# Performance work log

Measured on AMD Instinct MI355X. Metric: run time of the kernel, lower is better.

## Reference

```python
import jax, jax.numpy as jnp
import numpy as np
import math

LOG_EPS = -1000.0   # matches LOG_EPS in the torch source
NEG = -1e9          # stand-in for -inf (grad-safe)
T_MIN, T_MAX = 0.1, 1.0
GUMBEL_RATIO = 0.5  # gumbel_temperature_ratio forward arg (scalar float)


def setup_inputs() -> dict:
    key = jax.random.key(0)
    k1, k2, k3 = jax.random.split(key, 3)
    B, I, J, D = 4, 96, 384, 256
    return {
        "text_embeddings": jax.random.normal(k1, (B, I, D), jnp.float32),
        "mel_embeddings": jax.random.normal(k2, (B, J, D), jnp.float32),
        "gumbel_noise_u": jax.random.uniform(k3, (B, I, J), jnp.float32,
                                             minval=1e-6, maxval=1.0 - 1e-6),
        "text_mask": jnp.ones((B, I), dtype=bool),
        "mel_mask": jnp.ones((B, J), dtype=bool),
    }


def _soft_alignment(text_embeddings, mel_embeddings, gumbel_noise_u, text_mask, mel_mask):
    B, I, Dt = text_embeddings.shape
    _, J, Dm = mel_embeddings.shape

    # energy (B, I, J) = bmm / sqrt(D_text * D_mel)
    energy = jnp.einsum('bid,bjd->bij', text_embeddings, mel_embeddings) / math.sqrt(Dt * Dm)
    # gumbel noise + temperature
    temperature = T_MIN + (T_MAX - T_MIN) * GUMBEL_RATIO
    noise = -jnp.log(-jnp.log(gumbel_noise_u))
    energy = (energy + noise) / temperature

    len_t = text_mask.sum(1)  # (B,)
    len_m = mel_mask.sum(1)   # (B,)
    j_idx = jnp.arange(J)

    # invalid triangular mask (B, I, J, K): boundary j must not precede previous boundary k
    tri = j_idx[:, None] < j_idx[None, :]                       # (J, K)
    invalid = (tri[None, None]
               | ~text_mask[:, :, None, None]
               | ~mel_mask[:, None, :, None]
               | ~mel_mask[:, None, None, :])
    # force_assign_last: last text token's boundary forced to the last mel frame
    last_i = jnp.arange(I)[None, :] == (len_t - 1)[:, None]     # (B, I)
    not_last_j = j_idx[None, :] != (len_m - 1)[:, None]         # (B, J)
    invalid = invalid | (last_i[:, :, None, None] & not_last_j[:, None, :, None])

    # log conditional prob P(B_i = j | B_{i-1} = k), normalized over j (axis=2)
    e4 = jnp.where(invalid, LOG_EPS, energy[..., None])         # (B, I, J, K)
    log_cond_prob = e4 - jax.nn.logsumexp(e4, axis=2, keepdims=True)
    # reverse logcumsumexp over j: log P(B_i >= j | B_{i-1} = k)
    geq = jnp.flip(jax.lax.cumlogsumexp(jnp.flip(log_cond_prob, 2), axis=2), 2)
    geq = jnp.where(invalid, LOG_EPS, geq)

    # forward DP: B_ij (B, I+1, J+1), B_ij[:,0,0] = 0
    row0 = jnp.full((B, J + 1), NEG).at[:, 0].set(0.0)
    jj = jnp.arange(1, J + 1)

    def step(prev, inp):
        i, lcp = inp                                            # lcp: (B, J, K=J)
        # B_ij[b,i,j] = lse_k B_ij[b,i-1,k] + log_cond_prob[b,i-1,j-1,k]
        vals = jax.nn.logsumexp(prev[:, None, :-1] + lcp, axis=2)  # (B, J)
        window = (jj >= i) & (jj <= J - I + i + 1)              # only j in [i, J-I+i+1] written
        new = jnp.where(window[None, :], vals, NEG)
        new = jnp.concatenate([jnp.full((B, 1), NEG), new], axis=1)
        return new, new

    _, rows = jax.lax.scan(step, row0,
                           (jnp.arange(1, I + 1), jnp.swapaxes(log_cond_prob, 0, 1)))
    Bij = jnp.concatenate([row0[:, None, :], jnp.swapaxes(rows, 0, 1)], axis=1)  # (B, I+1, J+1)

    prob = Bij[:, :-1, :-1]                                     # (B, I, K)
    # log P(B_{i-1} < j <= B_i) = lse_k prob[b,i,k] + geq[b,i,j,k]
    log_boundary = jax.nn.logsumexp(prob[:, :, None, :] + geq, axis=3)  # (B, I, J)
    return log_boundary


def reference(text_embeddings, mel_embeddings, gumbel_noise_u, text_mask, mel_mask):
    soft = _soft_alignment(text_embeddings, mel_embeddings, gumbel_noise_u,
                           text_mask, mel_mask)
    # expanded text embeddings (B, J, D_text)
    expanded = jnp.einsum('bij,bid->bjd', jnp.exp(soft), text_embeddings)
    return soft, expanded
```

## Files before the change

### kernel.cpp

```cpp
#include <hip/hip_runtime.h>
#include <hip/hip_bf16.h>
#include <math.h>

#define B_ 4
#define I_ 96
#define J_ 384
#define D_ 256
#define NEG_     -1000000000.0f
#define NEGINF_  -3.0e38f
#define INV_TEMP_ (1.0f/0.55f)
#define LOG2E_   1.4426950408889634f
#define LN2_     0.6931471805599453f
#define LOGEPS2_ (-1000.0f*LOG2E_)

__device__ __forceinline__ float lse2(float a, float b) {
    float m = fmaxf(a, b);
    float d = fminf(a, b) - m;
    return m + __log2f(1.0f + __builtin_exp2f(d));
}

template<int CTRL, int RMASK = 0xF>
__device__ __forceinline__ float dpp_mv(float x, float fill) {
    return __int_as_float(__builtin_amdgcn_update_dpp(
        __float_as_int(fill), __float_as_int(x), CTRL, RMASK, 0xF, false));
}
template<int CTRL, int RMASK = 0xF>
__device__ __forceinline__ float dpp_id(float x) { return dpp_mv<CTRL,RMASK>(x, NEGINF_); }
__device__ __forceinline__ float rdlane(float x, int l_const) {
    return __int_as_float(__builtin_amdgcn_readlane(__float_as_int(x), l_const));
}

__device__ __forceinline__ void pcomb(float& m, float& s, float om, float os) {
    float d  = om - m;
    float e  = __builtin_exp2f(-__builtin_fabsf(d));
    float sh = (d > 0.0f) ? os : s;
    float sl = (d > 0.0f) ? s  : os;
    s = __builtin_fmaf(sl, e, sh);
    m = fmaxf(m, om);
}
__device__ __forceinline__ void wave_prefix_pair(float& m, float& s) {
    { float om=dpp_mv<0x111>(m,NEGINF_), os=dpp_mv<0x111>(s,0.f); pcomb(m,s,om,os); }
    { float om=dpp_mv<0x112>(m,NEGINF_), os=dpp_mv<0x112>(s,0.f); pcomb(m,s,om,os); }
    { float om=dpp_mv<0x114>(m,NEGINF_), os=dpp_mv<0x114>(s,0.f); pcomb(m,s,om,os); }
    { float om=dpp_mv<0x118>(m,NEGINF_), os=dpp_mv<0x118>(s,0.f); pcomb(m,s,om,os); }
    { float om=dpp_mv<0x142,0xa>(m,NEGINF_), os=dpp_mv<0x142,0xa>(s,0.f); pcomb(m,s,om,os); }
    { float om=dpp_mv<0x143,0xc>(m,NEGINF_), os=dpp_mv<0x143,0xc>(s,0.f); pcomb(m,s,om,os); }
}

__device__ __forceinline__ float wave_incl_prefix_lse(float x) {
    x = lse2(x, dpp_id<0x111>(x));
    x = lse2(x, dpp_id<0x112>(x));
    x = lse2(x, dpp_id<0x114>(x));
    x = lse2(x, dpp_id<0x118>(x));
    x = lse2(x, dpp_id<0x142, 0xa>(x));
    x = lse2(x, dpp_id<0x143, 0xc>(x));
    return x;
}
__device__ __forceinline__ float wave_incl_suffix_lse(float x, int lane) {
    x = lse2(x, dpp_id<0x101>(x));
    x = lse2(x, dpp_id<0x102>(x));
    x = lse2(x, dpp_id<0x104>(x));
    x = lse2(x, dpp_id<0x108>(x));
    float t1 = rdlane(x, 16), t2 = rdlane(x, 32), t3 = rdlane(x, 48);
    int row = lane >> 4;
    float u23 = lse2(t2, t3);
    float add = (row == 3) ? NEGINF_ : (row == 2) ? t3
              : (row == 1) ? u23 : lse2(t1, u23);
    return lse2(x, add);
}
__device__ __forceinline__ float combine_pre(const float* p, int w) {
    float l01 = lse2(p[0], p[1]);
    float l23 = lse2(p[2], p[3]);
    float P3 = lse2(l01, p[2]);
    float P4 = lse2(l01, l23);
    float P5 = lse2(P4, p[4]);
    return (w == 0) ? NEGINF_ : (w == 1) ? p[0] : (w == 2) ? l01
         : (w == 3) ? P3 : (w == 4) ? P4 : P5;
}
__device__ __forceinline__ float combine_suf(const float* s, int w) {
    float h45 = lse2(s[4], s[5]);
    float h23 = lse2(s[2], s[3]);
    float S3 = lse2(s[3], h45);
    float S2 = lse2(h23, h45);
    float S1 = lse2(s[1], S2);
    return (w == 5) ? NEGINF_ : (w == 4) ? s[5] : (w == 3) ? h45
         : (w == 2) ? S3 : (w == 1) ? S2 : S1;
}

__global__ __launch_bounds__(384) void k_energy(
    const float* __restrict__ text, const float* __restrict__ mel,
    const float* __restrict__ gum, float* __restrict__ Sarr,
    float* __restrict__ Earr)
{
    const int ib = blockIdx.x * 6, b = blockIdx.y;
    const int tid = threadIdx.x, lane = tid & 63, w = tid >> 6;
    __shared__ float4 tex4[6][D_/4];
    __shared__ float e2l[6][J_];

    {
        int r = tid >> 6, c = tid & 63;
        tex4[r][c] = ((const float4*)(text + ((size_t)b*I_ + ib + r)*D_))[c];
    }
    __syncthreads();

    const int j = tid;
    const float4* mrow = (const float4*)(mel + ((size_t)b*J_ + j)*D_);
    float acc[6] = {0.f,0.f,0.f,0.f,0.f,0.f};
    #pragma unroll 4
    for (int d4 = 0; d4 < D_/4; ++d4) {
        float4 m4 = mrow[d4];
        #pragma unroll
        for (int r = 0; r < 6; ++r) {
            float4 t4 = tex4[r][d4];
            acc[r] += t4.x*m4.x + t4.y*m4.y + t4.z*m4.z + t4.w*m4.w;
        }
    }
    #pragma unroll
    for (int r = 0; r < 6; ++r) {
        float u = gum[((size_t)b*I_ + ib + r)*J_ + j];
        float noise = -__logf(-__logf(u));
        e2l[r][j] = (acc[r] * (1.0f/256.0f) + noise) * (INV_TEMP_ * LOG2E_);
    }
    __syncthreads();

    const int k0 = lane * 6;
    float x[6];
    #pragma unroll
    for (int t = 0; t < 6; ++t) x[t] = e2l[w][k0 + t];
    float s1[6], s2[6], sfx[6];
    #pragma unroll
    for (int t = 0; t < 5; ++t) s1[t] = lse2(x[t], x[t+1]);
    s1[5] = x[5];
    #pragma unroll
    for (int t = 0; t < 4; ++t) s2[t] = lse2(s1[t], s1[t+2]);
    s2[4] = s1[4]; s2[5] = s1[5];
    sfx[0] = lse2(s2[0], s2[4]);
    sfx[1] = lse2(s2[1], s2[5]);
    #pragma unroll
    for (int t = 2; t < 6; ++t) sfx[t] = s2[t];
    float incl = wave_incl_suffix_lse(sfx[0], lane);
    float excl = dpp_id<0x130>(incl);
    size_t rowoff = ((size_t)b*I_ + ib + w)*J_ + k0;
    #pragma unroll
    for (int t = 0; t < 6; ++t) {
        Sarr[rowoff + t] = lse2(sfx[t], excl);
        Earr[rowoff + t] = x[t];
    }
}

__global__ __launch_bounds__(64) void k_dp(
    const float* __restrict__ Sarr, const float* __restrict__ Earr,
    float* __restrict__ prob)
{
    const int b = blockIdx.x;
    const int lane = threadIdx.x;
    const int k0 = lane * 6;
    const float* Sb = Sarr + (size_t)b*I_*J_;
    const float* Eb = Earr + (size_t)b*I_*J_;
    float* Pb = prob + (size_t)b*I_*J_;

    float prev[6];
    #pragma unroll
    for (int t = 0; t < 6; ++t) {
        int k = k0 + t;
        float v0 = (k == 0) ? 0.0f : NEG_;
        prev[t] = v0;
        Pb[k] = v0;
    }
    float SA[6], EA[6], SBf[6], EBf[6];
    #pragma unroll
    for (int t = 0; t < 6; ++t) {
        int k = k0 + t;
        SA[t] = Sb[k];
        EA[t] = Eb[(k == 0) ? 0 : k - 1];
    }
    #pragma unroll
    for (int t = 0; t < 6; ++t) {
        int k = k0 + t;
        SBf[t] = Sb[(size_t)1*J_ + k];
        EBf[t] = Eb[(size_t)1*J_ + ((k == 0) ? 0 : k - 1)];
    }

    auto STEP = [&](int i, float* Sx, float* Ex, int loadrow) {
        float v[6], E6[6];
        #pragma unroll
        for (int t = 0; t < 6; ++t) { v[t] = prev[t] - Sx[t]; E6[t] = Ex[t]; }
        if (loadrow >= 0) {
            #pragma unroll
            for (int t = 0; t < 6; ++t) {
                int k = k0 + t;
                Sx[t] = Sb[(size_t)loadrow*J_ + k];
                Ex[t] = Eb[(size_t)loadrow*J_ + ((k == 0) ? 0 : k - 1)];
            }
        }
        float qm[6], qs[6];
        qm[0] = v[0]; qs[0] = 1.0f;
        #pragma unroll
        for (int t = 1; t < 6; ++t) { qm[t] = v[t]; qs[t] = 1.0f; pcomb(qm[t], qs[t], v[t-1], 1.0f); }
        float rm[6], rs[6];
        rm[0] = qm[0]; rs[0] = qs[0]; rm[1] = qm[1]; rs[1] = qs[1];
        #pragma unroll
        for (int t = 2; t < 6; ++t) { rm[t] = qm[t]; rs[t] = qs[t]; pcomb(rm[t], rs[t], qm[t-2], qs[t-2]); }
        float fm[6], fs[6];
        #pragma unroll
        for (int t = 0; t < 4; ++t) { fm[t] = rm[t]; fs[t] = rs[t]; }
        fm[4] = rm[4]; fs[4] = rs[4]; pcomb(fm[4], fs[4], rm[0], rs[0]);
        fm[5] = rm[5]; fs[5] = rs[5]; pcomb(fm[5], fs[5], rm[1], rs[1]);
        float Lm = fm[5], Ls = fs[5];
        wave_prefix_pair(Lm, Ls);
        float pexm = dpp_mv<0x138>(Lm, NEGINF_);
        float pexs = dpp_mv<0x138>(Ls, 0.0f);
        float nv[6];
        nv[0] = pexm + __log2f(pexs) + E6[0];
        #pragma unroll
        for (int t = 1; t < 6; ++t) {
            float cm = pexm, cs = pexs;
            pcomb(cm, cs, fm[t-1], fs[t-1]);
            nv[t] = cm + __log2f(cs) + E6[t];
        }
        float* Prow = Pb + (size_t)i*J_;
        #pragma unroll
        for (int t = 0; t < 6; ++t) {
            int k = k0 + t;
            bool win = (k >= i) && (k <= 289 + i);
            float val = win ? nv[t] : NEG_;
            prev[t] = val;
            Prow[k] = val;
        }
    };

    int i = 1;
    for (; i + 1 <= I_-1; i += 2) {
        STEP(i,     SA,  EA,  (i + 1 <= I_-2) ? i + 1 : -1);
        STEP(i + 1, SBf, EBf, (i + 2 <= I_-2) ? i + 2 : -1);
    }
    if (i == I_-1) STEP(i, SA, EA, -1);
}

__global__ __launch_bounds__(384) void k_soft(
    float* __restrict__ probsoft,
    const float* __restrict__ Sarr)
{
    const int i = blockIdx.x, b = blockIdx.y;
    const int tid = threadIdx.x, lane = tid & 63, w = tid >> 6;
    const int j = tid;
    __shared__ float tot[12];
    float* Row = probsoft + ((size_t)b*I_ + i)*J_;
    float p = Row[j];

    if (i == I_-1) {
        float sincl = wave_incl_suffix_lse(p, lane);
        if (lane == 0) tot[w] = sincl;
        __syncthreads();
        float m = tot[0];
        #pragma unroll
        for (int t = 1; t < 6; ++t) m = lse2(m, tot[t]);
        Row[j] = (j == J_-1) ? LN2_ * m : LN2_ * m - 1000.0f;
        return;
    }

    float S6 = Sarr[((size_t)b*I_ + i)*J_ + j];
    float v = p - S6;
    float qincl = wave_incl_prefix_lse(v);
    float tsuf  = wave_incl_suffix_lse(p, lane);
    if (lane == 63) tot[w] = qincl;
    if (lane == 0)  tot[6 + w] = tsuf;
    __syncthreads();
    float pt[6], st[6];
    #pragma unroll
    for (int t = 0; t < 6; ++t) { pt[t] = tot[t]; st[t] = tot[6+t]; }
    float Qful = lse2(combine_pre(pt, w), qincl);
    float Texw = dpp_id<0x130>(tsuf);
    float Texc = lse2(combine_suf(st, w), Texw);
    Row[j] = LN2_ * lse2(Qful + S6, Texc + LOGEPS2_);
}

__global__ __launch_bounds__(256) void k_expand(
    const float* __restrict__ soft, const float* __restrict__ text,
    float* __restrict__ out2)
{
    const int jb = blockIdx.x * 8, b = blockIdx.y;
    const int tid = threadIdx.x;
    __shared__ float wsh[8][I_];
    for (int n = tid; n < 8*I_; n += 256) {
        int jj = n / I_, ii = n % I_;
        wsh[jj][ii] = __expf(soft[((size_t)b*I_ + ii)*J_ + jb + jj]);
    }
    __syncthreads();
    float acc[8] = {0.f,0.f,0.f,0.f,0.f,0.f,0.f,0.f};
    const float* tcol = text + (size_t)b*I_*D_ + tid;
    #pragma unroll 4
    for (int ii = 0; ii < I_; ++ii) {
        float tv = tcol[(size_t)ii*D_];
        #pragma unroll
        for (int jj = 0; jj < 8; ++jj) acc[jj] += wsh[jj][ii] * tv;
    }
    #pragma unroll
    for (int jj = 0; jj < 8; ++jj)
        out2[((size_t)b*J_ + jb + jj)*D_ + tid] = acc[jj];
}

extern "C" void kernel_launch(void* const* d_in, const int* in_sizes, int n_in,
                              void* d_out, int out_size, void* d_ws, size_t ws_size,
                              hipStream_t stream) {
    const float* text = (const float*)d_in[0];
    const float* mel  = (const float*)d_in[1];
    const float* gum  = (const float*)d_in[2];

    float* out    = (float*)d_out;
    float* soft   = out;
    float* out2   = out + (size_t)B_*I_*J_;
    float* Sarr   = out2;
    float* Earr   = out2 + (size_t)B_*I_*J_;
    float* prob   = soft;

    k_energy<<<dim3(I_/6, B_), 384, 0, stream>>>(text, mel, gum, Sarr, Earr);
    k_dp    <<<dim3(B_),        64, 0, stream>>>(Sarr, Earr, prob);
    k_soft  <<<dim3(I_, B_),   384, 0, stream>>>(prob, Sarr);
    k_expand<<<dim3(J_/8, B_), 256, 0, stream>>>(soft, text, out2);
}
```

Before: 163.6 us.

## Fuse DP recursion and soft-boundary pass into one kernel with LDS-resident probabilities

Merges the single-wave DP kernel and the per-row soft-alignment kernel into one 384-thread block per batch. The full probability table (96x384 floats) stays in shared memory, which removes a kernel launch and the global write/read round-trip of the prob rows. Wave 0 runs the DP while the other waves idle; after a barrier all six waves compute the soft output, 16 rows each. The DP scan also switches from a (max, scaled-sum) pair combine to plain pairwise log-sum-exp, which needs a log per combine but carries fewer values. The soft phase now runs on only 4 blocks instead of 384, so that work is serialized.

```diff
diff --git a/kernel.cpp b/kernel.cpp
--- a/kernel.cpp
+++ b/kernel.cpp
@@ -20,31 +20,12 @@
 }
 
 template<int CTRL, int RMASK = 0xF>
-__device__ __forceinline__ float dpp_mv(float x, float fill) {
+__device__ __forceinline__ float dpp_id(float x) {
     return __int_as_float(__builtin_amdgcn_update_dpp(
-        __float_as_int(fill), __float_as_int(x), CTRL, RMASK, 0xF, false));
-}
-template<int CTRL, int RMASK = 0xF>
-__device__ __forceinline__ float dpp_id(float x) { return dpp_mv<CTRL,RMASK>(x, NEGINF_); }
+        __float_as_int(NEGINF_), __float_as_int(x), CTRL, RMASK, 0xF, false));
+}
 __device__ __forceinline__ float rdlane(float x, int l_const) {
     return __int_as_float(__builtin_amdgcn_readlane(__float_as_int(x), l_const));
-}
-
-__device__ __forceinline__ void pcomb(float& m, float& s, float om, float os) {
-    float d  = om - m;
-    float e  = __builtin_exp2f(-__builtin_fabsf(d));
-    float sh = (d > 0.0f) ? os : s;
-    float sl = (d > 0.0f) ? s  : os;
-    s = __builtin_fmaf(sl, e, sh);
-    m = fmaxf(m, om);
-}
-__device__ __forceinline__ void wave_prefix_pair(float& m, float& s) {
-    { float om=dpp_mv<0x111>(m,NEGINF_), os=dpp_mv<0x111>(s,0.f); pcomb(m,s,om,os); }
-    { float om=dpp_mv<0x112>(m,NEGINF_), os=dpp_mv<0x112>(s,0.f); pcomb(m,s,om,os); }
-    { float om=dpp_mv<0x114>(m,NEGINF_), os=dpp_mv<0x114>(s,0.f); pcomb(m,s,om,os); }
-    { float om=dpp_mv<0x118>(m,NEGINF_), os=dpp_mv<0x118>(s,0.f); pcomb(m,s,om,os); }
-    { float om=dpp_mv<0x142,0xa>(m,NEGINF_), os=dpp_mv<0x142,0xa>(s,0.f); pcomb(m,s,om,os); }
-    { float om=dpp_mv<0x143,0xc>(m,NEGINF_), os=dpp_mv<0x143,0xc>(s,0.f); pcomb(m,s,om,os); }
 }
 
 __device__ __forceinline__ float wave_incl_prefix_lse(float x) {
@@ -68,24 +49,6 @@
               : (row == 1) ? u23 : lse2(t1, u23);
     return lse2(x, add);
 }
-__device__ __forceinline__ float combine_pre(const float* p, int w) {
-    float l01 = lse2(p[0], p[1]);
-    float l23 = lse2(p[2], p[3]);
-    float P3 = lse2(l01, p[2]);
-    float P4 = lse2(l01, l23);
-    float P5 = lse2(P4, p[4]);
-    return (w == 0) ? NEGINF_ : (w == 1) ? p[0] : (w == 2) ? l01
-         : (w == 3) ? P3 : (w == 4) ? P4 : P5;
-}
-__device__ __forceinline__ float combine_suf(const float* s, int w) {
-    float h45 = lse2(s[4], s[5]);
-    float h23 = lse2(s[2], s[3]);
-    float S3 = lse2(s[3], h45);
-    float S2 = lse2(h23, h45);
-    float S1 = lse2(s[1], S2);
-    return (w == 5) ? NEGINF_ : (w == 4) ? s[5] : (w == 3) ? h45
-         : (w == 2) ? S3 : (w == 1) ? S2 : S1;
-}
 
 __global__ __launch_bounds__(384) void k_energy(
     const float* __restrict__ text, const float* __restrict__ mel,
@@ -148,131 +111,154 @@
     }
 }
 
-__global__ __launch_bounds__(64) void k_dp(
+__global__ __launch_bounds__(384) void k_dpsoft(
     const float* __restrict__ Sarr, const float* __restrict__ Earr,
-    float* __restrict__ prob)
+    float* __restrict__ soft)
 {
+    __shared__ float probL[I_*J_];
     const int b = blockIdx.x;
-    const int lane = threadIdx.x;
+    const int tid = threadIdx.x, lane = tid & 63, w = tid >> 6;
     const int k0 = lane * 6;
     const float* Sb = Sarr + (size_t)b*I_*J_;
-    const float* Eb = Earr + (size_t)b*I_*J_;
-    float* Pb = prob + (size_t)b*I_*J_;
-
-    float prev[6];
-    #pragma unroll
-    for (int t = 0; t < 6; ++t) {
-        int k = k0 + t;
-        float v0 = (k == 0) ? 0.0f : NEG_;
-        prev[t] = v0;
-        Pb[k] = v0;
-    }
-    float SA[6], EA[6], SBf[6], EBf[6];
-    #pragma unroll
-    for (int t = 0; t < 6; ++t) {
-        int k = k0 + t;
-        SA[t] = Sb[k];
-        EA[t] = Eb[(k == 0) ? 0 : k - 1];
-    }
-    #pragma unroll
-    for (int t = 0; t < 6; ++t) {
-        int k = k0 + t;
-        SBf[t] = Sb[(size_t)1*J_ + k];
-        EBf[t] = Eb[(size_t)1*J_ + ((k == 0) ? 0 : k - 1)];
-    }
-
-    auto STEP = [&](int i, float* Sx, float* Ex, int loadrow) {
-        float v[6], E6[6];
-        #pragma unroll
-        for (int t = 0; t < 6; ++t) { v[t] = prev[t] - Sx[t]; E6[t] = Ex[t]; }
-        if (loadrow >= 0) {
+
+    if (w == 0) {
+        const float* Eb = Earr + (size_t)b*I_*J_;
+        float prev[6];
+        #pragma unroll
+        for (int t = 0; t < 6; ++t) {
+            int k = k0 + t;
+            float v0 = (k == 0) ? 0.0f : NEG_;
+            prev[t] = v0;
+            probL[k] = v0;
+        }
+        float SA[6], EA[6], SBf[6], EBf[6];
+        #pragma unroll
+        for (int t = 0; t < 6; ++t) {
+            int k = k0 + t;
+            SA[t] = Sb[k];
+            EA[t] = Eb[(k == 0) ? 0 : k - 1];
+        }
+        #pragma unroll
+        for (int t = 0; t < 6; ++t) {
+            int k = k0 + t;
+            SBf[t] = Sb[(size_t)1*J_ + k];
+            EBf[t] = Eb[(size_t)1*J_ + ((k == 0) ? 0 : k - 1)];
+        }
+        auto STEP = [&](int i, float* Sx, float* Ex, int loadrow) {
+            float v[6], E6[6];
+            #pragma unroll
+            for (int t = 0; t < 6; ++t) { v[t] = prev[t] - Sx[t]; E6[t] = Ex[t]; }
+            if (loadrow >= 0) {
+                #pragma unroll
+                for (int t = 0; t < 6; ++t) {
+                    int k = k0 + t;
+                    Sx[t] = Sb[(size_t)loadrow*J_ + k];
+                    Ex[t] = Eb[(size_t)loadrow*J_ + ((k == 0) ? 0 : k - 1)];
+                }
+            }
+            float p1[6], p2[6], p[6];
+            p1[0] = v[0];
+            #pragma unroll
+            for (int t = 1; t < 6; ++t) p1[t] = lse2(v[t-1], v[t]);
+            p2[0] = p1[0]; p2[1] = p1[1];
+            #pragma unroll
+            for (int t = 2; t < 6; ++t) p2[t] = lse2(p1[t-2], p1[t]);
+            p[0] = p2[0]; p[1] = p2[1]; p[2] = p2[2]; p[3] = p2[3];
+            p[4] = lse2(p2[0], p2[4]);
+            p[5] = lse2(p2[1], p2[5]);
+            float inc = wave_incl_prefix_lse(p[5]);
+            float pexcl = dpp_id<0x138>(inc);
+            float nv[6];
+            nv[0] = pexcl + E6[0];
+            #pragma unroll
+            for (int t = 1; t < 6; ++t) nv[t] = lse2(pexcl, p[t-1]) + E6[t];
+            float* Prow = probL + (size_t)i*J_;
             #pragma unroll
             for (int t = 0; t < 6; ++t) {
                 int k = k0 + t;
-                Sx[t] = Sb[(size_t)loadrow*J_ + k];
-                Ex[t] = Eb[(size_t)loadrow*J_ + ((k == 0) ? 0 : k - 1)];
+                bool win = (k >= i) && (k <= 289 + i);
+                float val = win ? nv[t] : NEG_;
+                prev[t] = val;
+                Prow[k] = val;
             }
-        }
-        float qm[6], qs[6];
-        qm[0] = v[0]; qs[0] = 1.0f;
-        #pragma unroll
-        for (int t = 1; t < 6; ++t) { qm[t] = v[t]; qs[t] = 1.0f; pcomb(qm[t], qs[t], v[t-1], 1.0f); }
-        float rm[6], rs[6];
-        rm[0] = qm[0]; rs[0] = qs[0]; rm[1] = qm[1]; rs[1] = qs[1];
-        #pragma unroll
-        for (int t = 2; t < 6; ++t) { rm[t] = qm[t]; rs[t] = qs[t]; pcomb(rm[t], rs[t], qm[t-2], qs[t-2]); }
-        float fm[6], fs[6];
-        #pragma unroll
-        for (int t = 0; t < 4; ++t) { fm[t] = rm[t]; fs[t] = rs[t]; }
-        fm[4] = rm[4]; fs[4] = rs[4]; pcomb(fm[4], fs[4], rm[0], rs[0]);
-        fm[5] = rm[5]; fs[5] = rs[5]; pcomb(fm[5], fs[5], rm[1], rs[1]);
-        float Lm = fm[5], Ls = fs[5];
-        wave_prefix_pair(Lm, Ls);
-        float pexm = dpp_mv<0x138>(Lm, NEGINF_);
-        float pexs = dpp_mv<0x138>(Ls, 0.0f);
-        float nv[6];
-        nv[0] = pexm + __log2f(pexs) + E6[0];
-        #pragma unroll
-        for (int t = 1; t < 6; ++t) {
-            float cm = pexm, cs = pexs;
-            pcomb(cm, cs, fm[t-1], fs[t-1]);
-            nv[t] = cm + __log2f(cs) + E6[t];
-        }
-        float* Prow = Pb + (size_t)i*J_;
-        #pragma unroll
-        for (int t = 0; t < 6; ++t) {
-            int k = k0 + t;
-            bool win = (k >= i) && (k <= 289 + i);
-            float val = win ? nv[t] : NEG_;
-            prev[t] = val;
-            Prow[k] = val;
-        }
-    };
-
-    int i = 1;
-    for (; i + 1 <= I_-1; i += 2) {
-        STEP(i,     SA,  EA,  (i + 1 <= I_-2) ? i + 1 : -1);
-        STEP(i + 1, SBf, EBf, (i + 2 <= I_-2) ? i + 2 : -1);
-    }
-    if (i == I_-1) STEP(i, SA, EA, -1);
-}
-
-__global__ __launch_bounds__(384) void k_soft(
-    float* __restrict__ probsoft,
-    const float* __restrict__ Sarr)
-{
-    const int i = blockIdx.x, b = blockIdx.y;
-    const int tid = threadIdx.x, lane = tid & 63, w = tid >> 6;
-    const int j = tid;
-    __shared__ float tot[12];
-    float* Row = probsoft + ((size_t)b*I_ + i)*J_;
-    float p = Row[j];
-
-    if (i == I_-1) {
-        float sincl = wave_incl_suffix_lse(p, lane);
-        if (lane == 0) tot[w] = sincl;
-        __syncthreads();
-        float m = tot[0];
-        #pragma unroll
-        for (int t = 1; t < 6; ++t) m = lse2(m, tot[t]);
-        Row[j] = (j == J_-1) ? LN2_ * m : LN2_ * m - 1000.0f;
-        return;
-    }
-
-    float S6 = Sarr[((size_t)b*I_ + i)*J_ + j];
-    float v = p - S6;
-    float qincl = wave_incl_prefix_lse(v);
-    float tsuf  = wave_incl_suffix_lse(p, lane);
-    if (lane == 63) tot[w] = qincl;
-    if (lane == 0)  tot[6 + w] = tsuf;
+        };
+        int i = 1;
+        for (; i + 1 <= I_-1; i += 2) {
+            STEP(i,     SA,  EA,  (i + 1 <= I_-2) ? i + 1 : -1);
+            STEP(i + 1, SBf, EBf, (i + 2 <= I_-2) ? i + 2 : -1);
+        }
+        if (i == I_-1) STEP(i, SA, EA, -1);
+    }
     __syncthreads();
-    float pt[6], st[6];
-    #pragma unroll
-    for (int t = 0; t < 6; ++t) { pt[t] = tot[t]; st[t] = tot[6+t]; }
-    float Qful = lse2(combine_pre(pt, w), qincl);
-    float Texw = dpp_id<0x130>(tsuf);
-    float Texc = lse2(combine_suf(st, w), Texw);
-    Row[j] = LN2_ * lse2(Qful + S6, Texc + LOGEPS2_);
+
+    float Scur[6], Snxt[6];
+    {
+        int i0 = w;
+        #pragma unroll
+        for (int t = 0; t < 6; ++t) Scur[t] = Sb[(size_t)i0*J_ + k0 + t];
+    }
+    for (int r = 0; r < 16; ++r) {
+        const int i = w + r * 6;
+        {
+            int inx = (r < 15) ? i + 6 : i;
+            #pragma unroll
+            for (int t = 0; t < 6; ++t) Snxt[t] = Sb[(size_t)inx*J_ + k0 + t];
+        }
+        float p6[6];
+        #pragma unroll
+        for (int t = 0; t < 6; ++t) p6[t] = probL[(size_t)i*J_ + k0 + t];
+
+        float* Row = soft + ((size_t)b*I_ + i)*J_ + k0;
+        if (i == I_-1) {
+            float tot_ = p6[0];
+            #pragma unroll
+            for (int t = 1; t < 6; ++t) tot_ = lse2(tot_, p6[t]);
+            float ws = wave_incl_suffix_lse(tot_, lane);
+            float m = rdlane(ws, 0);
+            #pragma unroll
+            for (int t = 0; t < 6; ++t) {
+                int j = k0 + t;
+                Row[t] = (j == J_-1) ? LN2_ * m : LN2_ * m - 1000.0f;
+            }
+        } else {
+            float v[6];
+            #pragma unroll
+            for (int t = 0; t < 6; ++t) v[t] = p6[t] - Scur[t];
+            float p1[6], p2[6], p[6];
+            p1[0] = v[0];
+            #pragma unroll
+            for (int t = 1; t < 6; ++t) p1[t] = lse2(v[t-1], v[t]);
+            p2[0] = p1[0]; p2[1] = p1[1];
+            #pragma unroll
+            for (int t = 2; t < 6; ++t) p2[t] = lse2(p1[t-2], p1[t]);
+            p[0] = p2[0]; p[1] = p2[1]; p[2] = p2[2]; p[3] = p2[3];
+            p[4] = lse2(p2[0], p2[4]);
+            p[5] = lse2(p2[1], p2[5]);
+            float inc = wave_incl_prefix_lse(p[5]);
+            float pexcl = dpp_id<0x138>(inc);
+            float s1[6], s2[6], ls[6];
+            #pragma unroll
+            for (int t = 0; t < 5; ++t) s1[t] = lse2(p6[t], p6[t+1]);
+            s1[5] = p6[5];
+            #pragma unroll
+            for (int t = 0; t < 4; ++t) s2[t] = lse2(s1[t], s1[t+2]);
+            s2[4] = s1[4]; s2[5] = s1[5];
+            ls[0] = lse2(s2[0], s2[4]);
+            ls[1] = lse2(s2[1], s2[5]);
+            #pragma unroll
+            for (int t = 2; t < 6; ++t) ls[t] = s2[t];
+            float wsuf = wave_incl_suffix_lse(ls[0], lane);
+            float wsx  = dpp_id<0x130>(wsuf);
+            #pragma unroll
+            for (int t = 0; t < 6; ++t) {
+                float Q = lse2(pexcl, p[t]);
+                float T = (t < 5) ? lse2(ls[t+1], wsx) : wsx;
+                Row[t] = LN2_ * lse2(Q + Scur[t], T + LOGEPS2_);
+            }
+        }
+        #pragma unroll
+        for (int t = 0; t < 6; ++t) Scur[t] = Snxt[t];
+    }
 }
 
 __global__ __launch_bounds__(256) void k_expand(
@@ -312,10 +298,8 @@
     float* out2   = out + (size_t)B_*I_*J_;
     float* Sarr   = out2;
     float* Earr   = out2 + (size_t)B_*I_*J_;
-    float* prob   = soft;
 
     k_energy<<<dim3(I_/6, B_), 384, 0, stream>>>(text, mel, gum, Sarr, Earr);
-    k_dp    <<<dim3(B_),        64, 0, stream>>>(Sarr, Earr, prob);
-    k_soft  <<<dim3(I_, B_),   384, 0, stream>>>(prob, Sarr);
+    k_dpsoft<<<dim3(B_),       384, 0, stream>>>(Sarr, Earr, soft);
     k_expand<<<dim3(J_/8, B_), 256, 0, stream>>>(soft, text, out2);
 }
```

After: 206.1 us. 26.0% more time.
